# Kernel optimization log

Measured on AMD Instinct MI355X. Metric: run time of the kernel, lower is better.

## Reference

```python
import jax, jax.numpy as jnp
import numpy as np
import math

B, S, E, H = 4, 2048, 1024, 16

def setup_inputs() -> dict:
    key = jax.random.key(0)
    k1, k2, k3 = jax.random.split(key, 3)
    scale_in = 1.0 / math.sqrt(E)
    x = jax.random.normal(k1, (B, S, E), dtype=jnp.float32)
    W_attn = jax.random.normal(k2, (E, 3 * E), dtype=jnp.float32) * scale_in
    b_attn = jnp.zeros((3 * E,), dtype=jnp.float32)
    W_proj = jax.random.normal(k3, (E, E), dtype=jnp.float32) * scale_in
    b_proj = jnp.zeros((E,), dtype=jnp.float32)
    return {"x": x, "W_attn": W_attn, "b_attn": b_attn, "W_proj": W_proj, "b_proj": b_proj}

def reference(x, W_attn, b_attn, W_proj, b_proj):
    batch, seq, emb = x.shape
    hd = emb // H  # head_dim
    qkv = x @ W_attn + b_attn                      # [B,S,3E]
    q, k, v = jnp.split(qkv, 3, axis=-1)
    # [B,S,E] -> [B,H,S,hd]
    q = q.reshape(batch, seq, H, hd).transpose(0, 2, 1, 3)
    k = k.reshape(batch, seq, H, hd).transpose(0, 2, 1, 3)
    v = v.reshape(batch, seq, H, hd).transpose(0, 2, 1, 3)
    scores = jnp.einsum('bhqd,bhkd->bhqk', q, k) * (1.0 / math.sqrt(hd))
    causal = jnp.tril(jnp.ones((seq, seq), dtype=bool))
    scores = jnp.where(causal[None, None, :, :], scores, jnp.finfo(scores.dtype).min)
    attn = jax.nn.softmax(scores, axis=-1)         # dropout p=0 -> identity
    out = jnp.einsum('bhqk,bhkd->bhqd', attn, v)   # [B,H,S,hd]
    out = out.transpose(0, 2, 1, 3).reshape(batch, seq, emb)
    return out @ W_proj + b_proj
```

## Files before the change

### kernel.cpp

```cpp
#include <hip/hip_runtime.h>

typedef __bf16 bf16;
typedef __bf16 bf16x8_t __attribute__((ext_vector_type(8)));
typedef __bf16 bf16x4_t __attribute__((ext_vector_type(4)));
typedef float f32x4_t __attribute__((ext_vector_type(4)));

#define S_ 2048
#define E_ 1024
#define HD 64
#define LOG2E 1.4426950408889634f
#define QSCALE (0.125f * LOG2E)

__device__ __forceinline__ void gl_lds16(const bf16* g, bf16* l) {
  __builtin_amdgcn_global_load_lds(
      (const __attribute__((address_space(1))) unsigned int*)g,
      (__attribute__((address_space(3))) unsigned int*)l, 16, 0, 0);
}

__device__ __forceinline__ void transpose_tile(const float* __restrict__ in,
                                               bf16* __restrict__ out,
                                               int R, int C, int bx, int by,
                                               float tile[32][33]) {
  int c0 = bx * 32, r0 = by * 32;
  int tx = threadIdx.x & 31, ty = threadIdx.x >> 5;
#pragma unroll
  for (int i = 0; i < 32; i += 8)
    tile[ty + i][tx] = in[(size_t)(r0 + ty + i) * C + c0 + tx];
  __syncthreads();
#pragma unroll
  for (int i = 0; i < 32; i += 8)
    out[(size_t)(c0 + ty + i) * R + r0 + tx] = (bf16)tile[tx][ty + i];
}

__global__ void prep(const float* __restrict__ x, bf16* __restrict__ xb,
                     const float* __restrict__ Wa, bf16* __restrict__ Wat,
                     const float* __restrict__ Wp, bf16* __restrict__ Wpt) {
  __shared__ float tile[32][33];
  int bid = blockIdx.x;
  if (bid < 8192) {
    int i = (bid * 256 + threadIdx.x) * 4;
    float4 v = *(const float4*)(x + i);
    bf16x4_t o = { (bf16)v.x, (bf16)v.y, (bf16)v.z, (bf16)v.w };
    *(bf16x4_t*)(xb + i) = o;
  } else if (bid < 8192 + 3072) {
    int f = bid - 8192;
    transpose_tile(Wa, Wat, 1024, 3072, f % 96, f / 96, tile);
  } else {
    int f = bid - 11264;
    transpose_tile(Wp, Wpt, 1024, 1024, f % 32, f / 32, tile);
  }
}

template <int MODE>
__global__ __launch_bounds__(256, 2)
void gemm128(const bf16* __restrict__ A, const bf16* __restrict__ Bt,
             const float* __restrict__ bias,
             bf16* __restrict__ Q, bf16* __restrict__ K, bf16* __restrict__ Vt,
             float* __restrict__ Out) {
  __shared__ __align__(16) bf16 As[128 * 64];
  __shared__ __align__(16) bf16 Bs[128 * 64];
  const int tid = threadIdx.x;
  const int wave = tid >> 6, lane = tid & 63;
  const int quad = lane >> 4, l16 = lane & 15;
  const int wm = wave >> 1, wn = wave & 1;
  const int bm = blockIdx.x, bn = blockIdx.y;

  f32x4_t acc[4][4];
#pragma unroll
  for (int i = 0; i < 4; i++)
#pragma unroll
    for (int j = 0; j < 4; j++) acc[i][j] = (f32x4_t){0.f, 0.f, 0.f, 0.f};

  for (int k0 = 0; k0 < 1024; k0 += 64) {
    __syncthreads();
#pragma unroll
    for (int it = 0; it < 4; it++) {
      int id = it * 256 + tid;
      int row = id >> 3, c = id & 7;
      int sc = (c ^ (row & 7)) * 8;
      gl_lds16(A + (size_t)(bm * 128 + row) * 1024 + k0 + sc, As + id * 8);
      gl_lds16(Bt + (size_t)(bn * 128 + row) * 1024 + k0 + sc, Bs + id * 8);
    }
    __syncthreads();
#pragma unroll
    for (int ks = 0; ks < 2; ks++) {
      bf16x8_t af[4], bfr[4];
#pragma unroll
      for (int i = 0; i < 4; i++) {
        int row = wm * 64 + i * 16 + l16;
        af[i] = *(const bf16x8_t*)&As[row * 64 + (((ks * 4 + quad) ^ (row & 7)) * 8)];
      }
#pragma unroll
      for (int j = 0; j < 4; j++) {
        int row = wn * 64 + j * 16 + l16;
        bfr[j] = *(const bf16x8_t*)&Bs[row * 64 + (((ks * 4 + quad) ^ (row & 7)) * 8)];
      }
#pragma unroll
      for (int i = 0; i < 4; i++)
#pragma unroll
        for (int j = 0; j < 4; j++)
          acc[i][j] = __builtin_amdgcn_mfma_f32_16x16x32_bf16(af[i], bfr[j], acc[i][j], 0, 0, 0);
    }
  }

  if (MODE == 0) {
#pragma unroll
    for (int j = 0; j < 4; j++) {
      int n_g = bn * 128 + wn * 64 + j * 16 + l16;
      float bv = bias[n_g];
      int which = n_g >> 10;
      int cc = n_g & 1023;
      int hh = cc >> 6, dd = cc & 63;
#pragma unroll
      for (int i = 0; i < 4; i++) {
        int m0 = bm * 128 + wm * 64 + i * 16 + quad * 4;
        int bb = m0 >> 11, ss0 = m0 & 2047;
        int bhn = bb * 16 + hh;
        if (which == 2) {
          bf16x4_t pk;
#pragma unroll
          for (int r = 0; r < 4; r++) pk[r] = (bf16)(acc[i][j][r] + bv);
          *(bf16x4_t*)&Vt[((size_t)bhn * 64 + dd) * 2048 + ss0] = pk;
        } else {
          bf16* dst = (which == 0) ? Q : K;
          float scl = (which == 0) ? QSCALE : 1.f;
#pragma unroll
          for (int r = 0; r < 4; r++)
            dst[((size_t)bhn * 2048 + ss0 + r) * 64 + dd] = (bf16)((acc[i][j][r] + bv) * scl);
        }
      }
    }
  } else {
#pragma unroll
    for (int j = 0; j < 4; j++) {
      int n_g = bn * 128 + wn * 64 + j * 16 + l16;
      float bv = bias[n_g];
#pragma unroll
      for (int i = 0; i < 4; i++) {
        int m0 = bm * 128 + wm * 64 + i * 16 + quad * 4;
#pragma unroll
        for (int r = 0; r < 4; r++)
          Out[(size_t)(m0 + r) * 1024 + n_g] = acc[i][j][r] + bv;
      }
    }
  }
}

__global__ __launch_bounds__(256, 2)
void attn_kernel(const bf16* __restrict__ Q, const bf16* __restrict__ K,
                 const bf16* __restrict__ Vt, bf16* __restrict__ O) {
  extern __shared__ __align__(16) bf16 smem[];
  bf16* Ks = smem;
  bf16* Vs = smem + 16384;
  bf16* Ps = smem + 32768;
  const int tid = threadIdx.x;
  const int wave = tid >> 6, lane = tid & 63;
  const int quad = lane >> 4, l16 = lane & 15;
  const int lin = blockIdx.y * 8 + blockIdx.x;
  const int w = (lin & 7) * 64 + (lin >> 3);
  const int pid = w & 7, bh = w >> 3;
  const int b = bh >> 4, h = bh & 15;

  const bf16* Qg = Q + (size_t)bh * S_ * HD;
  const bf16* Kg = K + (size_t)bh * S_ * HD;
  const bf16* Vg = Vt + (size_t)bh * HD * S_;
  bf16* Pw = Ps + wave * 2048;

  auto stage = [&](int c, int kb) {
    const bf16* Ksrc = Kg + (size_t)kb * 128 * HD;
    const bf16* Vsrc = Vg + kb * 128;
    bf16* Kd = Ks + c * 8192;
    bf16* Vd = Vs + c * 8192;
#pragma unroll
    for (int it = 0; it < 4; it++) {
      int id = it * 256 + tid;
      {
        int row = id >> 3, cc = id & 7;
        gl_lds16(Ksrc + row * 64 + ((cc ^ (row & 7)) * 8), Kd + id * 8);
      }
      {
        int d = id >> 4, cc = id & 15;
        gl_lds16(Vsrc + (size_t)d * S_ + ((cc ^ (d & 7)) * 8), Vd + id * 8);
      }
    }
  };

  int cur = 0;
  stage(0, 0);

  for (int qi = 0; qi < 2; qi++) {
    const int qb = qi ? (15 - pid) : pid;
    bf16x8_t qf[2][2];
#pragma unroll
    for (int ni = 0; ni < 2; ni++)
#pragma unroll
      for (int ks = 0; ks < 2; ks++)
        qf[ni][ks] = *(const bf16x8_t*)(Qg +
            (size_t)(qb * 128 + wave * 32 + ni * 16 + l16) * HD + ks * 32 + quad * 8);

    f32x4_t o[4][2];
#pragma unroll
    for (int mi = 0; mi < 4; mi++)
#pragma unroll
      for (int ni = 0; ni < 2; ni++) o[mi][ni] = (f32x4_t){0.f, 0.f, 0.f, 0.f};
    float m_[2] = {-1e30f, -1e30f}, l_[2] = {0.f, 0.f};

    if (qi == 0) __syncthreads();

    for (int kb = 0; kb <= qb; kb++) {
      if (kb < qb) stage(cur ^ 1, kb + 1);
      else if (qi == 0) stage(cur ^ 1, 0);

      const bf16* Kc = Ks + cur * 8192;
      const bf16* Vc = Vs + cur * 8192;

      f32x4_t sacc[8][2];
#pragma unroll
      for (int mi = 0; mi < 8; mi++)
#pragma unroll
        for (int ni = 0; ni < 2; ni++) sacc[mi][ni] = (f32x4_t){0.f, 0.f, 0.f, 0.f};
#pragma unroll
      for (int ks = 0; ks < 2; ks++)
#pragma unroll
        for (int mi = 0; mi < 8; mi++) {
          int kr = mi * 16 + l16;
          bf16x8_t kf = *(const bf16x8_t*)&Kc[kr * 64 + (((ks * 4 + quad) ^ (kr & 7)) * 8)];
          sacc[mi][0] = __builtin_amdgcn_mfma_f32_16x16x32_bf16(kf, qf[0][ks], sacc[mi][0], 0, 0, 0);
          sacc[mi][1] = __builtin_amdgcn_mfma_f32_16x16x32_bf16(kf, qf[1][ks], sacc[mi][1], 0, 0, 0);
        }

      if (kb == qb) {
#pragma unroll
        for (int mi = 0; mi < 8; mi++)
#pragma unroll
          for (int ni = 0; ni < 2; ni++) {
            int qrow = wave * 32 + ni * 16 + l16;
            int krow = mi * 16 + quad * 4;
#pragma unroll
            for (int r = 0; r < 4; r++)
              if (krow + r > qrow) sacc[mi][ni][r] = -1e30f;
          }
      }

#pragma unroll
      for (int ni = 0; ni < 2; ni++) {
        float mx = sacc[0][ni][0];
#pragma unroll
        for (int mi = 0; mi < 8; mi++)
#pragma unroll
          for (int r = 0; r < 4; r++) mx = fmaxf(mx, sacc[mi][ni][r]);
        mx = fmaxf(mx, __shfl_xor(mx, 16));
        mx = fmaxf(mx, __shfl_xor(mx, 32));
        float mnew = fmaxf(m_[ni], mx);
        float alpha = __builtin_amdgcn_exp2f(m_[ni] - mnew);
        m_[ni] = mnew;
        float rs = 0.f;
#pragma unroll
        for (int mi = 0; mi < 8; mi++)
#pragma unroll
          for (int r = 0; r < 4; r++) {
            float p = __builtin_amdgcn_exp2f(sacc[mi][ni][r] - mnew);
            sacc[mi][ni][r] = p;
            rs += p;
          }
        rs += __shfl_xor(rs, 16);
        rs += __shfl_xor(rs, 32);
        l_[ni] = alpha * l_[ni] + rs;
#pragma unroll
        for (int mi = 0; mi < 4; mi++)
#pragma unroll
          for (int r = 0; r < 4; r++) o[mi][ni][r] *= alpha;
      }

#pragma unroll
      for (int hh = 0; hh < 2; hh++) {
#pragma unroll
        for (int ni = 0; ni < 2; ni++) {
          int qr = ni * 16 + l16;
#pragma unroll
          for (int mm = 0; mm < 4; mm++) {
            bf16x4_t pk;
#pragma unroll
            for (int r = 0; r < 4; r++) pk[r] = (bf16)sacc[hh * 4 + mm][ni][r];
            int c = mm * 2 + (quad >> 1);
            *(bf16x4_t*)&Pw[qr * 64 + ((c ^ (qr & 7)) * 8) + (quad & 1) * 4] = pk;
          }
        }
#pragma unroll
        for (int k2 = 0; k2 < 2; k2++) {
          int ks2 = hh * 2 + k2;
          bf16x8_t vb[4], pa[2];
#pragma unroll
          for (int mi = 0; mi < 4; mi++) {
            int d = mi * 16 + l16;
            vb[mi] = *(const bf16x8_t*)&Vc[d * 128 + (((ks2 * 4 + quad) ^ (d & 7)) * 8)];
          }
#pragma unroll
          for (int ni = 0; ni < 2; ni++) {
            int qr = ni * 16 + l16;
            pa[ni] = *(const bf16x8_t*)&Pw[qr * 64 + (((k2 * 4 + quad) ^ (qr & 7)) * 8)];
          }
#pragma unroll
          for (int mi = 0; mi < 4; mi++)
#pragma unroll
            for (int ni = 0; ni < 2; ni++)
              o[mi][ni] = __builtin_amdgcn_mfma_f32_16x16x32_bf16(vb[mi], pa[ni], o[mi][ni], 0, 0, 0);
        }
      }

      __syncthreads();
      cur ^= 1;
    }

#pragma unroll
    for (int ni = 0; ni < 2; ni++) {
      float inv = 1.0f / l_[ni];
      int q_g = qb * 128 + wave * 32 + ni * 16 + l16;
      size_t rowb = (size_t)(b * S_ + q_g) * E_ + h * HD;
#pragma unroll
      for (int mi = 0; mi < 4; mi++) {
        bf16x4_t ov;
#pragma unroll
        for (int r = 0; r < 4; r++) ov[r] = (bf16)(o[mi][ni][r] * inv);
        *(bf16x4_t*)&O[rowb + mi * 16 + quad * 4] = ov;
      }
    }
  }
}

extern "C" void kernel_launch(void* const* d_in, const int* in_sizes, int n_in,
                              void* d_out, int out_size, void* d_ws, size_t ws_size,
                              hipStream_t stream) {
  const float* x      = (const float*)d_in[0];
  const float* W_attn = (const float*)d_in[1];
  const float* b_attn = (const float*)d_in[2];
  const float* W_proj = (const float*)d_in[3];
  const float* b_proj = (const float*)d_in[4];
  float* out = (float*)d_out;

  bf16* xb  = (bf16*)d_ws;
  bf16* Wat = xb + 8388608ull;
  bf16* Wpt = Wat + 3145728ull;
  bf16* Qb  = Wpt + 1048576ull;
  bf16* Kb  = Qb + 8388608ull;
  bf16* Vtb = Kb + 8388608ull;
  bf16* AOb = xb;

  prep<<<12288, 256, 0, stream>>>(x, xb, W_attn, Wat, W_proj, Wpt);
  gemm128<0><<<dim3(64, 24), 256, 0, stream>>>(xb, Wat, b_attn, Qb, Kb, Vtb, nullptr);
  attn_kernel<<<dim3(8, 64), 256, 81920, stream>>>(Qb, Kb, Vtb, AOb);
  gemm128<1><<<dim3(64, 8), 256, 0, stream>>>(AOb, Wpt, b_proj, nullptr, nullptr, nullptr, out);
}
```

Before: 230.0 us.

## Keep softmax probabilities in registers for PV MFMA instead of LDS round-trip

The P matrix is no longer written to shared memory and read back. The S-accumulator register layout is reused directly as the B operand of the PV MFMA, and the matching V elements are gathered with two 4-wide LDS reads per fragment. This removes the per-wave LDS staging buffer, cutting shared memory from 80KB to 64KB, which may allow more blocks per CU. The row max and row sum reductions are also vectorised, and the block-index swizzle is replaced by direct blockIdx mapping, which can change L2 locality.

```diff
diff --git a/kernel.cpp b/kernel.cpp
--- a/kernel.cpp
+++ b/kernel.cpp
@@ -15,6 +15,13 @@
   __builtin_amdgcn_global_load_lds(
       (const __attribute__((address_space(1))) unsigned int*)g,
       (__attribute__((address_space(3))) unsigned int*)l, 16, 0, 0);
+}
+
+__device__ __forceinline__ f32x4_t vmax4(f32x4_t a, f32x4_t b) {
+  f32x4_t r;
+  r[0] = fmaxf(a[0], b[0]); r[1] = fmaxf(a[1], b[1]);
+  r[2] = fmaxf(a[2], b[2]); r[3] = fmaxf(a[3], b[3]);
+  return r;
 }
 
 __device__ __forceinline__ void transpose_tile(const float* __restrict__ in,
@@ -152,19 +159,15 @@
   extern __shared__ __align__(16) bf16 smem[];
   bf16* Ks = smem;
   bf16* Vs = smem + 16384;
-  bf16* Ps = smem + 32768;
   const int tid = threadIdx.x;
   const int wave = tid >> 6, lane = tid & 63;
   const int quad = lane >> 4, l16 = lane & 15;
-  const int lin = blockIdx.y * 8 + blockIdx.x;
-  const int w = (lin & 7) * 64 + (lin >> 3);
-  const int pid = w & 7, bh = w >> 3;
+  const int pid = blockIdx.x, bh = blockIdx.y;
   const int b = bh >> 4, h = bh & 15;
 
   const bf16* Qg = Q + (size_t)bh * S_ * HD;
   const bf16* Kg = K + (size_t)bh * S_ * HD;
   const bf16* Vg = Vt + (size_t)bh * HD * S_;
-  bf16* Pw = Ps + wave * 2048;
 
   auto stage = [&](int c, int kb) {
     const bf16* Ksrc = Kg + (size_t)kb * 128 * HD;
@@ -244,25 +247,30 @@
 
 #pragma unroll
       for (int ni = 0; ni < 2; ni++) {
-        float mx = sacc[0][ni][0];
-#pragma unroll
-        for (int mi = 0; mi < 8; mi++)
-#pragma unroll
-          for (int r = 0; r < 4; r++) mx = fmaxf(mx, sacc[mi][ni][r]);
+        f32x4_t t0 = vmax4(vmax4(sacc[0][ni], sacc[1][ni]),
+                           vmax4(sacc[2][ni], sacc[3][ni]));
+        f32x4_t t1 = vmax4(vmax4(sacc[4][ni], sacc[5][ni]),
+                           vmax4(sacc[6][ni], sacc[7][ni]));
+        t0 = vmax4(t0, t1);
+        float mx = fmaxf(fmaxf(t0[0], t0[1]), fmaxf(t0[2], t0[3]));
         mx = fmaxf(mx, __shfl_xor(mx, 16));
         mx = fmaxf(mx, __shfl_xor(mx, 32));
         float mnew = fmaxf(m_[ni], mx);
         float alpha = __builtin_amdgcn_exp2f(m_[ni] - mnew);
         m_[ni] = mnew;
-        float rs = 0.f;
-#pragma unroll
-        for (int mi = 0; mi < 8; mi++)
+        f32x4_t a0 = {0.f, 0.f, 0.f, 0.f}, a1 = {0.f, 0.f, 0.f, 0.f};
+#pragma unroll
+        for (int mi = 0; mi < 4; mi++) {
 #pragma unroll
           for (int r = 0; r < 4; r++) {
-            float p = __builtin_amdgcn_exp2f(sacc[mi][ni][r] - mnew);
-            sacc[mi][ni][r] = p;
-            rs += p;
+            sacc[mi][ni][r] = __builtin_amdgcn_exp2f(sacc[mi][ni][r] - mnew);
+            sacc[mi + 4][ni][r] = __builtin_amdgcn_exp2f(sacc[mi + 4][ni][r] - mnew);
           }
+          a0 += sacc[mi][ni];
+          a1 += sacc[mi + 4][ni];
+        }
+        a0 += a1;
+        float rs = (a0[0] + a0[1]) + (a0[2] + a0[3]);
         rs += __shfl_xor(rs, 16);
         rs += __shfl_xor(rs, 32);
         l_[ni] = alpha * l_[ni] + rs;
@@ -273,38 +281,27 @@
       }
 
 #pragma unroll
-      for (int hh = 0; hh < 2; hh++) {
-#pragma unroll
-        for (int ni = 0; ni < 2; ni++) {
-          int qr = ni * 16 + l16;
-#pragma unroll
-          for (int mm = 0; mm < 4; mm++) {
-            bf16x4_t pk;
-#pragma unroll
-            for (int r = 0; r < 4; r++) pk[r] = (bf16)sacc[hh * 4 + mm][ni][r];
-            int c = mm * 2 + (quad >> 1);
-            *(bf16x4_t*)&Pw[qr * 64 + ((c ^ (qr & 7)) * 8) + (quad & 1) * 4] = pk;
+      for (int f = 0; f < 4; f++) {
+        bf16x8_t pb[2];
+#pragma unroll
+        for (int ni = 0; ni < 2; ni++)
+#pragma unroll
+          for (int r = 0; r < 4; r++) {
+            pb[ni][r]     = (bf16)sacc[2 * f][ni][r];
+            pb[ni][r + 4] = (bf16)sacc[2 * f + 1][ni][r];
           }
-        }
-#pragma unroll
-        for (int k2 = 0; k2 < 2; k2++) {
-          int ks2 = hh * 2 + k2;
-          bf16x8_t vb[4], pa[2];
-#pragma unroll
-          for (int mi = 0; mi < 4; mi++) {
-            int d = mi * 16 + l16;
-            vb[mi] = *(const bf16x8_t*)&Vc[d * 128 + (((ks2 * 4 + quad) ^ (d & 7)) * 8)];
-          }
-#pragma unroll
-          for (int ni = 0; ni < 2; ni++) {
-            int qr = ni * 16 + l16;
-            pa[ni] = *(const bf16x8_t*)&Pw[qr * 64 + (((k2 * 4 + quad) ^ (qr & 7)) * 8)];
-          }
-#pragma unroll
-          for (int mi = 0; mi < 4; mi++)
-#pragma unroll
-            for (int ni = 0; ni < 2; ni++)
-              o[mi][ni] = __builtin_amdgcn_mfma_f32_16x16x32_bf16(vb[mi], pa[ni], o[mi][ni], 0, 0, 0);
+#pragma unroll
+        for (int mi = 0; mi < 4; mi++) {
+          int d = mi * 16 + l16;
+          int e = d & 7;
+          int g1 = 4 * f + (quad >> 1);
+          const bf16* rp = Vc + d * 128 + (quad & 1) * 4;
+          bf16x4_t lo = *(const bf16x4_t*)(rp + ((g1 ^ e) * 8));
+          bf16x4_t hi = *(const bf16x4_t*)(rp + (((g1 + 2) ^ e) * 8));
+          bf16x8_t vb = __builtin_shufflevector(lo, hi, 0, 1, 2, 3, 4, 5, 6, 7);
+#pragma unroll
+          for (int ni = 0; ni < 2; ni++)
+            o[mi][ni] = __builtin_amdgcn_mfma_f32_16x16x32_bf16(vb, pb[ni], o[mi][ni], 0, 0, 0);
         }
       }
 
@@ -348,6 +345,6 @@
 
   prep<<<12288, 256, 0, stream>>>(x, xb, W_attn, Wat, W_proj, Wpt);
   gemm128<0><<<dim3(64, 24), 256, 0, stream>>>(xb, Wat, b_attn, Qb, Kb, Vtb, nullptr);
-  attn_kernel<<<dim3(8, 64), 256, 81920, stream>>>(Qb, Kb, Vtb, AOb);
+  attn_kernel<<<dim3(8, 64), 256, 65536, stream>>>(Qb, Kb, Vtb, AOb);
   gemm128<1><<<dim3(64, 8), 256, 0, stream>>>(AOb, Wpt, b_proj, nullptr, nullptr, nullptr, out);
 }
```

New measurement: 238.5 us. +3.7%, slower.

## Stage QKV GEMM epilogue through LDS for coalesced 16-byte stores; simplify attention block mapping

Applied to the files above, without the earlier changes.

The QKV projection epilogue now writes bias-added, scaled bf16 results into a swizzled LDS scratch tile, then reads it back so each thread issues 16-byte vector stores to Q, K and the transposed V. This replaces scattered 2-byte stores (Q/K) and 8-byte strided stores (Vt) with contiguous writes. It costs extra LDS traffic and two barriers per block. The attention kernel also drops its remapped block index in favour of direct blockIdx mapping, which changes block scheduling order and L2 locality.

```diff
diff --git a/kernel.cpp b/kernel.cpp
--- a/kernel.cpp
+++ b/kernel.cpp
@@ -57,8 +57,9 @@
              const float* __restrict__ bias,
              bf16* __restrict__ Q, bf16* __restrict__ K, bf16* __restrict__ Vt,
              float* __restrict__ Out) {
-  __shared__ __align__(16) bf16 As[128 * 64];
-  __shared__ __align__(16) bf16 Bs[128 * 64];
+  __shared__ __align__(16) bf16 smem_g[2 * 128 * 64];
+  bf16* As = smem_g;
+  bf16* Bs = smem_g + 8192;
   const int tid = threadIdx.x;
   const int wave = tid >> 6, lane = tid & 63;
   const int quad = lane >> 4, l16 = lane & 15;
@@ -104,30 +105,60 @@
   }
 
   if (MODE == 0) {
-#pragma unroll
-    for (int j = 0; j < 4; j++) {
-      int n_g = bn * 128 + wn * 64 + j * 16 + l16;
-      float bv = bias[n_g];
-      int which = n_g >> 10;
-      int cc = n_g & 1023;
-      int hh = cc >> 6, dd = cc & 63;
-#pragma unroll
-      for (int i = 0; i < 4; i++) {
-        int m0 = bm * 128 + wm * 64 + i * 16 + quad * 4;
-        int bb = m0 >> 11, ss0 = m0 & 2047;
-        int bhn = bb * 16 + hh;
-        if (which == 2) {
+    __syncthreads();
+    bf16* scr = smem_g;
+    const int which = bn >> 3;
+    if (which < 2) {
+      const float scl = (which == 0) ? QSCALE : 1.f;
+#pragma unroll
+      for (int j = 0; j < 4; j++) {
+        int n_l = wn * 64 + j * 16 + l16;
+        float bv = bias[bn * 128 + n_l];
+#pragma unroll
+        for (int i = 0; i < 4; i++)
+#pragma unroll
+          for (int r = 0; r < 4; r++) {
+            int m = wm * 64 + i * 16 + quad * 4 + r;
+            scr[m * 128 + (((n_l >> 3) ^ (m & 7)) * 8) + (n_l & 7)] =
+                (bf16)((acc[i][j][r] + bv) * scl);
+          }
+      }
+      __syncthreads();
+      bf16* dst0 = (which == 0) ? Q : K;
+#pragma unroll
+      for (int it = 0; it < 8; it++) {
+        int g = it * 256 + tid;
+        int m = g >> 4, c16 = g & 15;
+        bf16x8_t v8 = *(const bf16x8_t*)&scr[m * 128 + ((c16 ^ (m & 7)) * 8)];
+        int m0 = bm * 128 + m;
+        int cc = (bn & 7) * 128 + c16 * 8;
+        int bhn = (m0 >> 11) * 16 + (cc >> 6);
+        *(bf16x8_t*)&dst0[((size_t)bhn * 2048 + (m0 & 2047)) * 64 + (cc & 63)] = v8;
+      }
+    } else {
+#pragma unroll
+      for (int j = 0; j < 4; j++) {
+        int n_l = wn * 64 + j * 16 + l16;
+        float bv = bias[bn * 128 + n_l];
+#pragma unroll
+        for (int i = 0; i < 4; i++) {
+          int mb = wm * 64 + i * 16 + quad * 4;
           bf16x4_t pk;
 #pragma unroll
           for (int r = 0; r < 4; r++) pk[r] = (bf16)(acc[i][j][r] + bv);
-          *(bf16x4_t*)&Vt[((size_t)bhn * 64 + dd) * 2048 + ss0] = pk;
-        } else {
-          bf16* dst = (which == 0) ? Q : K;
-          float scl = (which == 0) ? QSCALE : 1.f;
-#pragma unroll
-          for (int r = 0; r < 4; r++)
-            dst[((size_t)bhn * 2048 + ss0 + r) * 64 + dd] = (bf16)((acc[i][j][r] + bv) * scl);
+          *(bf16x4_t*)&scr[n_l * 128 + (((mb >> 3) ^ (n_l & 7)) * 8) + (mb & 7)] = pk;
         }
+      }
+      __syncthreads();
+#pragma unroll
+      for (int it = 0; it < 8; it++) {
+        int g = it * 256 + tid;
+        int n_l = g >> 4, c16 = g & 15;
+        bf16x8_t v8 = *(const bf16x8_t*)&scr[n_l * 128 + ((c16 ^ (n_l & 7)) * 8)];
+        int m0 = bm * 128 + c16 * 8;
+        int cc = (bn & 7) * 128 + n_l;
+        int bhn = (m0 >> 11) * 16 + (cc >> 6);
+        *(bf16x8_t*)&Vt[((size_t)bhn * 64 + (cc & 63)) * 2048 + (m0 & 2047)] = v8;
       }
     }
   } else {
@@ -156,9 +187,7 @@
   const int tid = threadIdx.x;
   const int wave = tid >> 6, lane = tid & 63;
   const int quad = lane >> 4, l16 = lane & 15;
-  const int lin = blockIdx.y * 8 + blockIdx.x;
-  const int w = (lin & 7) * 64 + (lin >> 3);
-  const int pid = w & 7, bh = w >> 3;
+  const int pid = blockIdx.x, bh = blockIdx.y;
   const int b = bh >> 4, h = bh & 15;
 
   const bf16* Qg = Q + (size_t)bh * S_ * HD;
```

Measured after the change: 243.2 us. +5.7%, slower.
